# Kernel optimization log

Measured on AMD Instinct MI355X. Metric: run time of the kernel, lower is better.

## Reference

```python
import jax, jax.numpy as jnp
import numpy as np

# Model dims (Gemma-class)
B, T, HID = 1, 3072, 2048
H, KH, D = 16, 8, 128          # q heads, kv heads, head_dim
WIN = 1024                     # sliding window
EPS = 1e-6
SEQ = 1536                     # two packed sequences of length 1536


def _rms(x, w):
    # torch nn.RMSNorm: x * rsqrt(mean(x^2) + eps) [* weight]
    var = jnp.mean(x * x, axis=-1, keepdims=True)
    y = x * jax.lax.rsqrt(var + EPS)
    return y if w is None else y * w


def _rotate_half(x):
    x1, x2 = jnp.split(x, 2, axis=-1)
    return jnp.concatenate([-x2, x1], axis=-1)


def _rope(x, cos, sin):
    # x: [B,T,h,D]; cos/sin: [B,T,rd] -> unsqueeze head dim (matches cos.unsqueeze(2))
    c = cos[:, :, None, :]
    s = sin[:, :, None, :]
    rd = cos.shape[-1]
    xr, xp = x[..., :rd], x[..., rd:]
    xr = xr * c + _rotate_half(xr) * s
    return jnp.concatenate([xr, xp], axis=-1)


def _build_mask(cu_seqlens):
    # causal & within sliding window & same packed sequence (matches _sliding_mask)
    idx = jnp.arange(T)
    seg = jnp.searchsorted(cu_seqlens, idx, side='right') - 1
    i = idx[:, None]
    j = idx[None, :]
    return (i >= j) & ((i - j) < WIN) & (seg[:, None] == seg[None, :])


def _attn_layer(x, wq, qn, k, v, wo, cos, sin, mask):
    # x: [B,T,HID]; k,v: [T,KH,D] (possibly shared from an earlier layer)
    q = _rope(_rms((x @ wq).reshape(B, T, H, D), qn), cos, sin).reshape(T, H, D)
    rep = H // k.shape[1]
    kk = jnp.repeat(k, rep, axis=1)   # GQA: repeat_interleave over head dim
    vv = jnp.repeat(v, rep, axis=1)
    s = jnp.einsum('qhd,khd->hqk', q, kk)          # scale = 1.0 (as in source)
    s = jnp.where(mask, s, jnp.asarray(-1e30, s.dtype))
    p = jax.nn.softmax(s, axis=-1)
    o = jnp.einsum('hqk,khd->qhd', p, vv).reshape(B, T, H * D)
    return o @ wo


def setup_inputs() -> dict:
    key = jax.random.key(0)
    ks = jax.random.split(key, 10)
    hidden_states = jax.random.normal(ks[0], (B, T, HID), jnp.float32)
    # RoPE tables with per-packed-sequence position resets
    pos = jnp.concatenate([jnp.arange(SEQ), jnp.arange(SEQ)]).astype(jnp.float32)
    inv = 1.0 / (10000.0 ** (jnp.arange(0, D, 2, dtype=jnp.float32) / D))
    fr = pos[:, None] * inv[None, :]
    emb = jnp.concatenate([fr, fr], axis=-1)     # [T, D]
    cos = jnp.cos(emb)[None]                     # [1, T, D]
    sin = jnp.sin(emb)[None]
    w = lambda k, sh: 0.02 * jax.random.normal(k, sh, jnp.float32)
    return {
        'hidden_states': hidden_states,
        'cos': cos, 'sin': sin,
        'wq0': w(ks[1], (HID, H * D)), 'wk0': w(ks[2], (HID, KH * D)),
        'wv0': w(ks[3], (HID, KH * D)), 'wo0': w(ks[4], (H * D, HID)),
        'qn0': 1.0 + 0.01 * jax.random.normal(ks[5], (D,), jnp.float32),
        'kn0': 1.0 + 0.01 * jax.random.normal(ks[6], (D,), jnp.float32),
        'wq1': w(ks[7], (HID, H * D)), 'wo1': w(ks[8], (H * D, HID)),
        'qn1': 1.0 + 0.01 * jax.random.normal(ks[9], (D,), jnp.float32),
        'cu_seqlens': jnp.array([0, SEQ, T], dtype=jnp.int32),
    }


def reference(hidden_states, cos, sin, wq0, wk0, wv0, wo0, qn0, kn0, wq1, wo1, qn1, cu_seqlens):
    mask = _build_mask(cu_seqlens)
    # Layer 0: source layer -> computes and stores K/V
    k = _rope(_rms((hidden_states @ wk0).reshape(B, T, KH, D), kn0), cos, sin).reshape(T, KH, D)
    v = _rms((hidden_states @ wv0).reshape(B, T, KH, D), None).reshape(T, KH, D)
    out0 = _attn_layer(hidden_states, wq0, qn0, k, v, wo0, cos, sin, mask)
    # Layer 1: KV-shared layer -> reuses layer 0's K/V (skips k/v projections)
    out1 = _attn_layer(out0, wq1, qn1, k, v, wo1, cos, sin, mask)
    return out1
```

## Files before the change

kernel.cpp:

```cpp
#include <hip/hip_runtime.h>
#include <hip/hip_bf16.h>

#define T_TOK 3072
#define HIDDEN 2048
#define NHQ 16
#define NHKV 8
#define DH 128
#define WINDOW 1024

typedef __attribute__((ext_vector_type(4))) float f32x4;
typedef __attribute__((ext_vector_type(8))) short bf16x8;
typedef __attribute__((ext_vector_type(8))) unsigned short ushort8;
typedef __attribute__((ext_vector_type(4))) unsigned short ushort4v;

__device__ __forceinline__ unsigned short f2bf(float f) {
  union { float fv; unsigned u; } v; v.fv = f;
  unsigned r = v.u + 0x7fffu + ((v.u >> 16) & 1u);
  return (unsigned short)(r >> 16);
}
__device__ __forceinline__ float bf2f(unsigned short h) {
  union { unsigned u; float f; } v; v.u = ((unsigned)h) << 16;
  return v.f;
}
__device__ __forceinline__ void split2(float f, unsigned short& hi, unsigned short& lo) {
  hi = f2bf(f);
  lo = f2bf(f - bf2f(hi));
}

__global__ __launch_bounds__(256) void cvt_split(const float* __restrict__ x,
                                                 unsigned short* __restrict__ yh,
                                                 unsigned short* __restrict__ yl, int n) {
  int i = (blockIdx.x * 256 + threadIdx.x) * 4;
  if (i >= n) return;
  f32x4 v = *(const f32x4*)(x + i);
  ushort4v oh, ol;
#pragma unroll
  for (int j = 0; j < 4; ++j) {
    unsigned short h, l;
    split2(v[j], h, l);
    oh[j] = h; ol[j] = l;
  }
  *(ushort4v*)(yh + i) = oh;
  *(ushort4v*)(yl + i) = ol;
}

__global__ __launch_bounds__(256) void transpose_w_split(const float* __restrict__ W,
                                                         unsigned short* __restrict__ Wth,
                                                         unsigned short* __restrict__ Wtl,
                                                         int K, int N) {
  __shared__ float tile[32][33];
  int bn = blockIdx.x * 32, bk = blockIdx.y * 32;
  int tx = threadIdx.x & 31, ty = threadIdx.x >> 5;
#pragma unroll
  for (int i = 0; i < 4; ++i)
    tile[ty + i * 8][tx] = W[(size_t)(bk + ty + i * 8) * N + bn + tx];
  __syncthreads();
#pragma unroll
  for (int i = 0; i < 4; ++i) {
    unsigned short h, l;
    split2(tile[tx][ty + i * 8], h, l);
    Wth[(size_t)(bn + ty + i * 8) * K + bk + tx] = h;
    if (Wtl) Wtl[(size_t)(bn + ty + i * 8) * K + bk + tx] = l;
  }
}

__global__ __launch_bounds__(256) void transpose_u16(const unsigned short* __restrict__ src,
                                                     unsigned short* __restrict__ dst,
                                                     int R, int C) {
  __shared__ unsigned short tile[32][33];
  int bc = blockIdx.x * 32, br = blockIdx.y * 32;
  int tx = threadIdx.x & 31, ty = threadIdx.x >> 5;
#pragma unroll
  for (int i = 0; i < 4; ++i)
    tile[ty + i * 8][tx] = src[(size_t)(br + ty + i * 8) * C + bc + tx];
  __syncthreads();
#pragma unroll
  for (int i = 0; i < 4; ++i)
    dst[(size_t)(bc + ty + i * 8) * R + br + tx] = tile[tx][ty + i * 8];
}

#define GSLOT(lane) ((((lane) & 3) + 4 - (((lane) >> 3) & 3)) & 3)

__global__ __launch_bounds__(256) void gemm3_128(const unsigned short* __restrict__ Ah,
                                                 const unsigned short* __restrict__ Al,
                                                 const unsigned short* __restrict__ Bh,
                                                 const unsigned short* __restrict__ Bl,
                                                 float* __restrict__ Cq,
                                                 float* __restrict__ Ckv,
                                                 int strd, int M, int N, int K) {
  __shared__ unsigned short ah_lds[128 * 32];
  __shared__ unsigned short al_lds[128 * 32];
  __shared__ unsigned short bh_lds[128 * 32];
  __shared__ unsigned short bl_lds[128 * 32];
  const int tid = threadIdx.x, lane = tid & 63, wave = tid >> 6;
  const int wr = (wave >> 1) * 64, wc = (wave & 1) * 64;
  const int g = lane >> 4, r16 = lane & 15;
  int nwg = gridDim.x * gridDim.y;
  int id = blockIdx.y * gridDim.x + blockIdx.x;
  int nid = (id & 7) * (nwg >> 3) + (id >> 3);
  const int bm = nid % gridDim.x, bn = nid / gridDim.x;
  f32x4 acc[4][4];
#pragma unroll
  for (int i = 0; i < 4; ++i)
#pragma unroll
    for (int j = 0; j < 4; ++j) acc[i][j] = (f32x4){0.f, 0.f, 0.f, 0.f};

  const unsigned short* AhB = Ah + (size_t)bm * 128 * K;
  const unsigned short* AlB = Al + (size_t)bm * 128 * K;
  const unsigned short* BhB = Bh + (size_t)bn * 128 * K;
  const unsigned short* BlB = Bl + (size_t)bn * 128 * K;

  const int slg = GSLOT(lane) * 8;
  const int sr = ((r16 >> 1) & 3);

  for (int kt = 0; kt < K; kt += 32) {
    __syncthreads();
#pragma unroll
    for (int c = 0; c < 2; ++c) {
      size_t goff = (size_t)(wave * 32 + c * 16 + (lane >> 2)) * K + kt + slg;
      int loff = (wave * 2 + c) * 512;
      __builtin_amdgcn_global_load_lds(
          (const __attribute__((address_space(1))) unsigned int*)(AhB + goff),
          (__attribute__((address_space(3))) unsigned int*)(ah_lds + loff), 16, 0, 0);
      __builtin_amdgcn_global_load_lds(
          (const __attribute__((address_space(1))) unsigned int*)(AlB + goff),
          (__attribute__((address_space(3))) unsigned int*)(al_lds + loff), 16, 0, 0);
      __builtin_amdgcn_global_load_lds(
          (const __attribute__((address_space(1))) unsigned int*)(BhB + goff),
          (__attribute__((address_space(3))) unsigned int*)(bh_lds + loff), 16, 0, 0);
      __builtin_amdgcn_global_load_lds(
          (const __attribute__((address_space(1))) unsigned int*)(BlB + goff),
          (__attribute__((address_space(3))) unsigned int*)(bl_lds + loff), 16, 0, 0);
    }
    __syncthreads();
    bf16x8 ahf[4], alf[4], bhf[4], blf[4];
#pragma unroll
    for (int i = 0; i < 4; ++i) {
      int sa = ((g + sr) & 3) * 8;
      ahf[i] = *(const bf16x8*)&ah_lds[(wr + i * 16 + r16) * 32 + sa];
      alf[i] = *(const bf16x8*)&al_lds[(wr + i * 16 + r16) * 32 + sa];
      bhf[i] = *(const bf16x8*)&bh_lds[(wc + i * 16 + r16) * 32 + sa];
      blf[i] = *(const bf16x8*)&bl_lds[(wc + i * 16 + r16) * 32 + sa];
    }
#pragma unroll
    for (int i = 0; i < 4; ++i)
#pragma unroll
      for (int j = 0; j < 4; ++j) {
        acc[i][j] = __builtin_amdgcn_mfma_f32_16x16x32_bf16(ahf[i], bhf[j], acc[i][j], 0, 0, 0);
        acc[i][j] = __builtin_amdgcn_mfma_f32_16x16x32_bf16(ahf[i], blf[j], acc[i][j], 0, 0, 0);
        acc[i][j] = __builtin_amdgcn_mfma_f32_16x16x32_bf16(alf[i], bhf[j], acc[i][j], 0, 0, 0);
      }
  }

#pragma unroll
  for (int i = 0; i < 4; ++i) {
    int row = bm * 128 + wr + i * 16 + g * 4;
#pragma unroll
    for (int j = 0; j < 4; ++j) {
      int colg = bn * 128 + wc + j * 16 + r16;
      float* Cb; int cc;
      if (colg < 2048) { Cb = Cq; cc = colg; } else { Cb = Ckv; cc = colg - 2048; }
#pragma unroll
      for (int r = 0; r < 4; ++r)
        Cb[(size_t)(row + r) * strd + cc] = acc[i][j][r];
    }
  }
}

template <int OUT>
__global__ __launch_bounds__(256) void gemm3_96(const unsigned short* __restrict__ Ah,
                                                const unsigned short* __restrict__ Al,
                                                const unsigned short* __restrict__ Bh,
                                                const unsigned short* __restrict__ Bl,
                                                float* __restrict__ Cf,
                                                unsigned short* __restrict__ Ch,
                                                unsigned short* __restrict__ Cl,
                                                int M, int N, int K) {
  __shared__ unsigned short ah_lds[96 * 32];
  __shared__ unsigned short al_lds[96 * 32];
  __shared__ unsigned short bh_lds[128 * 32];
  __shared__ unsigned short bl_lds[128 * 32];
  const int tid = threadIdx.x, lane = tid & 63, wave = tid >> 6;
  const int wr = (wave >> 1) * 48, wc = (wave & 1) * 64;
  const int g = lane >> 4, r16 = lane & 15;
  int nwg = gridDim.x * gridDim.y;
  int id = blockIdx.y * gridDim.x + blockIdx.x;
  int nid = (id & 7) * (nwg >> 3) + (id >> 3);
  const int bm = nid % gridDim.x, bn = nid / gridDim.x;
  f32x4 acc[3][4];
#pragma unroll
  for (int i = 0; i < 3; ++i)
#pragma unroll
    for (int j = 0; j < 4; ++j) acc[i][j] = (f32x4){0.f, 0.f, 0.f, 0.f};

  const unsigned short* AhB = Ah + (size_t)bm * 96 * K;
  const unsigned short* AlB = Al + (size_t)bm * 96 * K;
  const unsigned short* BhB = Bh + (size_t)bn * 128 * K;
  const unsigned short* BlB = Bl + (size_t)bn * 128 * K;

  const int slg = GSLOT(lane) * 8;
  const int sr = ((r16 >> 1) & 3);

  for (int kt = 0; kt < K; kt += 32) {
    __syncthreads();
    {
      int c = wave;
      size_t goff = (size_t)(c * 16 + (lane >> 2)) * K + kt + slg;
      __builtin_amdgcn_global_load_lds(
          (const __attribute__((address_space(1))) unsigned int*)(AhB + goff),
          (__attribute__((address_space(3))) unsigned int*)(ah_lds + c * 512), 16, 0, 0);
      __builtin_amdgcn_global_load_lds(
          (const __attribute__((address_space(1))) unsigned int*)(AlB + goff),
          (__attribute__((address_space(3))) unsigned int*)(al_lds + c * 512), 16, 0, 0);
      if (wave < 2) {
        int c2 = 4 + wave;
        size_t goff2 = (size_t)(c2 * 16 + (lane >> 2)) * K + kt + slg;
        __builtin_amdgcn_global_load_lds(
            (const __attribute__((address_space(1))) unsigned int*)(AhB + goff2),
            (__attribute__((address_space(3))) unsigned int*)(ah_lds + c2 * 512), 16, 0, 0);
        __builtin_amdgcn_global_load_lds(
            (const __attribute__((address_space(1))) unsigned int*)(AlB + goff2),
            (__attribute__((address_space(3))) unsigned int*)(al_lds + c2 * 512), 16, 0, 0);
      }
    }
#pragma unroll
    for (int c = 0; c < 2; ++c) {
      size_t goff = (size_t)(wave * 32 + c * 16 + (lane >> 2)) * K + kt + slg;
      int loff = (wave * 2 + c) * 512;
      __builtin_amdgcn_global_load_lds(
          (const __attribute__((address_space(1))) unsigned int*)(BhB + goff),
          (__attribute__((address_space(3))) unsigned int*)(bh_lds + loff), 16, 0, 0);
      __builtin_amdgcn_global_load_lds(
          (const __attribute__((address_space(1))) unsigned int*)(BlB + goff),
          (__attribute__((address_space(3))) unsigned int*)(bl_lds + loff), 16, 0, 0);
    }
    __syncthreads();
    bf16x8 ahf[3], alf[3], bhf[4], blf[4];
    int sa = ((g + sr) & 3) * 8;
#pragma unroll
    for (int i = 0; i < 3; ++i) {
      ahf[i] = *(const bf16x8*)&ah_lds[(wr + i * 16 + r16) * 32 + sa];
      alf[i] = *(const bf16x8*)&al_lds[(wr + i * 16 + r16) * 32 + sa];
    }
#pragma unroll
    for (int j = 0; j < 4; ++j) {
      bhf[j] = *(const bf16x8*)&bh_lds[(wc + j * 16 + r16) * 32 + sa];
      blf[j] = *(const bf16x8*)&bl_lds[(wc + j * 16 + r16) * 32 + sa];
    }
#pragma unroll
    for (int i = 0; i < 3; ++i)
#pragma unroll
      for (int j = 0; j < 4; ++j) {
        acc[i][j] = __builtin_amdgcn_mfma_f32_16x16x32_bf16(ahf[i], bhf[j], acc[i][j], 0, 0, 0);
        acc[i][j] = __builtin_amdgcn_mfma_f32_16x16x32_bf16(ahf[i], blf[j], acc[i][j], 0, 0, 0);
        acc[i][j] = __builtin_amdgcn_mfma_f32_16x16x32_bf16(alf[i], bhf[j], acc[i][j], 0, 0, 0);
      }
  }

#pragma unroll
  for (int i = 0; i < 3; ++i) {
    int row = bm * 96 + wr + i * 16 + g * 4;
#pragma unroll
    for (int j = 0; j < 4; ++j) {
      int col = bn * 128 + wc + j * 16 + r16;
#pragma unroll
      for (int r = 0; r < 4; ++r) {
        if (OUT == 0) {
          Cf[(size_t)(row + r) * N + col] = acc[i][j][r];
        } else {
          unsigned short h, l;
          split2(acc[i][j][r], h, l);
          Ch[(size_t)(row + r) * N + col] = h;
          Cl[(size_t)(row + r) * N + col] = l;
        }
      }
    }
  }
}

__global__ __launch_bounds__(256) void gemm1_96(const unsigned short* __restrict__ Ah,
                                                const unsigned short* __restrict__ Bh,
                                                float* __restrict__ Cf,
                                                int M, int N, int K) {
  __shared__ unsigned short ah_lds[96 * 32];
  __shared__ unsigned short bh_lds[128 * 32];
  const int tid = threadIdx.x, lane = tid & 63, wave = tid >> 6;
  const int wr = (wave >> 1) * 48, wc = (wave & 1) * 64;
  const int g = lane >> 4, r16 = lane & 15;
  int nwg = gridDim.x * gridDim.y;
  int id = blockIdx.y * gridDim.x + blockIdx.x;
  int nid = (id & 7) * (nwg >> 3) + (id >> 3);
  const int bm = nid % gridDim.x, bn = nid / gridDim.x;
  f32x4 acc[3][4];
#pragma unroll
  for (int i = 0; i < 3; ++i)
#pragma unroll
    for (int j = 0; j < 4; ++j) acc[i][j] = (f32x4){0.f, 0.f, 0.f, 0.f};

  const unsigned short* AhB = Ah + (size_t)bm * 96 * K;
  const unsigned short* BhB = Bh + (size_t)bn * 128 * K;

  const int slg = GSLOT(lane) * 8;
  const int sr = ((r16 >> 1) & 3);

  for (int kt = 0; kt < K; kt += 32) {
    __syncthreads();
    {
      int c = wave;
      size_t goff = (size_t)(c * 16 + (lane >> 2)) * K + kt + slg;
      __builtin_amdgcn_global_load_lds(
          (const __attribute__((address_space(1))) unsigned int*)(AhB + goff),
          (__attribute__((address_space(3))) unsigned int*)(ah_lds + c * 512), 16, 0, 0);
      if (wave < 2) {
        int c2 = 4 + wave;
        size_t goff2 = (size_t)(c2 * 16 + (lane >> 2)) * K + kt + slg;
        __builtin_amdgcn_global_load_lds(
            (const __attribute__((address_space(1))) unsigned int*)(AhB + goff2),
            (__attribute__((address_space(3))) unsigned int*)(ah_lds + c2 * 512), 16, 0, 0);
      }
    }
#pragma unroll
    for (int c = 0; c < 2; ++c) {
      size_t goff = (size_t)(wave * 32 + c * 16 + (lane >> 2)) * K + kt + slg;
      __builtin_amdgcn_global_load_lds(
          (const __attribute__((address_space(1))) unsigned int*)(BhB + goff),
          (__attribute__((address_space(3))) unsigned int*)(bh_lds + (wave * 2 + c) * 512), 16, 0, 0);
    }
    __syncthreads();
    bf16x8 ahf[3], bhf[4];
    int sa = ((g + sr) & 3) * 8;
#pragma unroll
    for (int i = 0; i < 3; ++i)
      ahf[i] = *(const bf16x8*)&ah_lds[(wr + i * 16 + r16) * 32 + sa];
#pragma unroll
    for (int j = 0; j < 4; ++j)
      bhf[j] = *(const bf16x8*)&bh_lds[(wc + j * 16 + r16) * 32 + sa];
#pragma unroll
    for (int i = 0; i < 3; ++i)
#pragma unroll
      for (int j = 0; j < 4; ++j)
        acc[i][j] = __builtin_amdgcn_mfma_f32_16x16x32_bf16(ahf[i], bhf[j], acc[i][j], 0, 0, 0);
  }

#pragma unroll
  for (int i = 0; i < 3; ++i) {
    int row = bm * 96 + wr + i * 16 + g * 4;
#pragma unroll
    for (int j = 0; j < 4; ++j) {
      int col = bn * 128 + wc + j * 16 + r16;
#pragma unroll
      for (int r = 0; r < 4; ++r)
        Cf[(size_t)(row + r) * N + col] = acc[i][j][r];
    }
  }
}

__global__ __launch_bounds__(256) void rms_rope_split(const float* __restrict__ X,
                                                      const float* __restrict__ w,
                                                      const float* __restrict__ cosp,
                                                      const float* __restrict__ sinp,
                                                      unsigned short* __restrict__ outh,
                                                      unsigned short* __restrict__ outl,
                                                      int NH, int doRope, int XS, int XO) {
  int row = blockIdx.x * 4 + (threadIdx.x >> 6);
  int lane = threadIdx.x & 63;
  int t = row / NH, hh_ = row % NH;
  const float* x = X + (size_t)t * XS + XO + (size_t)hh_ * DH;
  float x1 = x[lane], x2 = x[lane + 64];
  float ss = x1 * x1 + x2 * x2;
#pragma unroll
  for (int m = 1; m < 64; m <<= 1) ss += __shfl_xor(ss, m, 64);
  float inv = rsqrtf(ss * (1.0f / 128.0f) + 1e-6f);
  float y1 = x1 * inv, y2 = x2 * inv;
  if (w) { y1 *= w[lane]; y2 *= w[lane + 64]; }
  if (doRope) {
    float c1 = cosp[t * DH + lane], s1 = sinp[t * DH + lane];
    float c2 = cosp[t * DH + lane + 64], s2 = sinp[t * DH + lane + 64];
    float o1 = y1 * c1 - y2 * s1;
    float o2 = y2 * c2 + y1 * s2;
    y1 = o1; y2 = o2;
  }
  unsigned short h, l;
  split2(y1, h, l);
  outh[(size_t)row * DH + lane] = h;
  if (outl) outl[(size_t)row * DH + lane] = l;
  split2(y2, h, l);
  outh[(size_t)row * DH + lane + 64] = h;
  if (outl) outl[(size_t)row * DH + lane + 64] = l;
}

template <int WRITE_LO>
__global__ __launch_bounds__(384) void attn3(const float* __restrict__ Qf,
                                             const float* __restrict__ qnw,
                                             const float* __restrict__ cosp,
                                             const float* __restrict__ sinp,
                                             const unsigned short* __restrict__ Kh,
                                             const unsigned short* __restrict__ Kl,
                                             const unsigned short* __restrict__ Vth,
                                             unsigned short* __restrict__ Oh,
                                             unsigned short* __restrict__ Ol,
                                             const int* __restrict__ cu, int ncu) {
  __shared__ unsigned short kh_lds[32][136];
  __shared__ unsigned short kl_lds[32][136];
  __shared__ unsigned short vh_lds[144][40];
  __shared__ unsigned short ph_lds[6][16][40];

  int id = blockIdx.y * gridDim.x + blockIdx.x;
  int nid = (id & 7) * 64 + (id >> 3);
  const int qt = nid & 31, h = nid >> 5;
  const int qbase = qt * 96;
  const int kvh = h >> 1;
  const int tid = threadIdx.x, lane = tid & 63, wave = tid >> 6;
  const int g = lane >> 4, r16 = lane & 15;

  for (int i = tid; i < 16 * 40; i += 384) {
    int rr = i / 40, cc = i % 40;
    vh_lds[128 + rr][cc] = (rr == 0) ? (unsigned short)0x3F80 : (unsigned short)0;
  }

  bf16x8 aqh[4], aql[4];
  {
    int q_r = qbase + wave * 16 + r16;
    const float* xq = Qf + (size_t)q_r * HIDDEN + h * DH;
    float xv[4][8];
    float ss = 0.f;
#pragma unroll
    for (int ks = 0; ks < 4; ++ks) {
      f32x4 a = *(const f32x4*)(xq + ks * 32 + g * 8);
      f32x4 b = *(const f32x4*)(xq + ks * 32 + g * 8 + 4);
#pragma unroll
      for (int j = 0; j < 4; ++j) { xv[ks][j] = a[j]; xv[ks][4 + j] = b[j]; }
#pragma unroll
      for (int j = 0; j < 8; ++j) ss += xv[ks][j] * xv[ks][j];
    }
    ss += __shfl_xor(ss, 16, 64);
    ss += __shfl_xor(ss, 32, 64);
    float inv = rsqrtf(ss * (1.0f / 128.0f) + 1e-6f);
    float y[4][8];
#pragma unroll
    for (int ks = 0; ks < 4; ++ks) {
      f32x4 w0 = *(const f32x4*)(qnw + ks * 32 + g * 8);
      f32x4 w1 = *(const f32x4*)(qnw + ks * 32 + g * 8 + 4);
#pragma unroll
      for (int j = 0; j < 4; ++j) {
        y[ks][j] = xv[ks][j] * inv * w0[j];
        y[ks][4 + j] = xv[ks][4 + j] * inv * w1[j];
      }
    }
    const float* cb = cosp + (size_t)q_r * DH;
    const float* sb = sinp + (size_t)q_r * DH;
#pragma unroll
    for (int ks = 0; ks < 4; ++ks) {
      bf16x8 th, tl;
#pragma unroll
      for (int j2 = 0; j2 < 2; ++j2) {
        int col = ks * 32 + g * 8 + j2 * 4;
        f32x4 cv = *(const f32x4*)(cb + col);
        f32x4 sv = *(const f32x4*)(sb + col);
#pragma unroll
        for (int j = 0; j < 4; ++j) {
          float o;
          if (ks < 2) o = y[ks][j2 * 4 + j] * cv[j] - y[ks + 2][j2 * 4 + j] * sv[j];
          else        o = y[ks][j2 * 4 + j] * cv[j] + y[ks - 2][j2 * 4 + j] * sv[j];
          unsigned short hx, lx;
          split2(o, hx, lx);
          th[j2 * 4 + j] = (short)hx;
          tl[j2 * 4 + j] = (short)lx;
        }
      }
      aqh[ks] = th; aql[ks] = tl;
    }
  }

  int ssr[4];
#pragma unroll
  for (int r = 0; r < 4; ++r) {
    int q_r = qbase + wave * 16 + g * 4 + r;
    int s = 0;
    for (int i = 1; i < ncu; ++i) { int v = cu[i]; if (v <= q_r) s = v; }
    ssr[r] = s;
  }
  int ss_base = 0;
  for (int i = 1; i < ncu; ++i) { int v = cu[i]; if (v <= qbase) ss_base = v; }

  float m_r[4] = {-1e30f, -1e30f, -1e30f, -1e30f};
  f32x4 oacc[8];
#pragma unroll
  for (int db = 0; db < 8; ++db) oacc[db] = (f32x4){0.f, 0.f, 0.f, 0.f};
  f32x4 oaccL = (f32x4){0.f, 0.f, 0.f, 0.f};

  int lo = qbase - WINDOW + 1;
  if (lo < ss_base) lo = ss_base;
  if (lo < 0) lo = 0;
  int kt0 = lo & ~31;
  int ktend = qbase + 95;

  const bool stager = tid < 256;
  const int krow = (tid & 255) >> 3, kc = tid & 7;
  const int vd = (tid & 255) >> 1, vhalf = (tid & 1) * 16;
  const int qmin = qbase + wave * 16;
  const int sw0 = ((kc + 2 * (krow & 15)) & 15) * 16;
  const int sw1 = ((kc + 8 + 2 * (krow & 15)) & 15) * 16;

  ushort8 rkh0, rkh1, rkl0, rkl1, rvh0, rvh1;
  auto loadTile = [&](int kt) {
    if (!stager) return;
    size_t goff = ((size_t)(kt + krow) * NHKV + kvh) * DH + kc * 8;
    rkh0 = *(const ushort8*)(Kh + goff);
    rkh1 = *(const ushort8*)(Kh + goff + 64);
    rkl0 = *(const ushort8*)(Kl + goff);
    rkl1 = *(const ushort8*)(Kl + goff + 64);
    size_t voff = ((size_t)kvh * DH + vd) * T_TOK + kt + vhalf;
    rvh0 = *(const ushort8*)(Vth + voff);
    rvh1 = *(const ushort8*)(Vth + voff + 8);
  };
  auto writeTile = [&]() {
    if (!stager) return;
    char* kbh = (char*)&kh_lds[krow][0];
    char* kbl = (char*)&kl_lds[krow][0];
    *(ushort8*)(kbh + sw0) = rkh0;
    *(ushort8*)(kbh + sw1) = rkh1;
    *(ushort8*)(kbl + sw0) = rkl0;
    *(ushort8*)(kbl + sw1) = rkl1;
    *(ushort8*)&vh_lds[vd][vhalf] = rvh0;
    *(ushort8*)&vh_lds[vd][vhalf + 8] = rvh1;
  };

  loadTile(kt0);
  writeTile();
  __syncthreads();

  for (int kt = kt0; kt <= ktend; kt += 32) {
    const bool hasNext = (kt + 32 <= ktend);
    if (hasNext) loadTile(kt + 32);

    f32x4 s0 = (f32x4){0.f, 0.f, 0.f, 0.f}, s1 = (f32x4){0.f, 0.f, 0.f, 0.f};
    {
      const char* kb0h = (const char*)&kh_lds[r16][0];
      const char* kb1h = (const char*)&kh_lds[16 + r16][0];
      const char* kb0l = (const char*)&kl_lds[r16][0];
      const char* kb1l = (const char*)&kl_lds[16 + r16][0];
#pragma unroll
      for (int ks = 0; ks < 4; ++ks) {
        int sl = ((ks * 4 + g + 2 * r16) & 15) * 16;
        bf16x8 bh0 = *(const bf16x8*)(kb0h + sl);
        bf16x8 bh1 = *(const bf16x8*)(kb1h + sl);
        bf16x8 bl0 = *(const bf16x8*)(kb0l + sl);
        bf16x8 bl1 = *(const bf16x8*)(kb1l + sl);
        s0 = __builtin_amdgcn_mfma_f32_16x16x32_bf16(aqh[ks], bh0, s0, 0, 0, 0);
        s0 = __builtin_amdgcn_mfma_f32_16x16x32_bf16(aqh[ks], bl0, s0, 0, 0, 0);
        s0 = __builtin_amdgcn_mfma_f32_16x16x32_bf16(aql[ks], bh0, s0, 0, 0, 0);
        s1 = __builtin_amdgcn_mfma_f32_16x16x32_bf16(aqh[ks], bh1, s1, 0, 0, 0);
        s1 = __builtin_amdgcn_mfma_f32_16x16x32_bf16(aqh[ks], bl1, s1, 0, 0, 0);
        s1 = __builtin_amdgcn_mfma_f32_16x16x32_bf16(aql[ks], bh1, s1, 0, 0, 0);
      }
    }

    float sv0_[4], sv1_[4], mt_[4];
    bool ok0_[4], ok1_[4];
    bool interior = (kt + 31 <= qmin) && (kt >= qmin + 16 - WINDOW) &&
                    __all(kt >= ssr[3]);
    if (interior) {
#pragma unroll
      for (int r = 0; r < 4; ++r) {
        ok0_[r] = ok1_[r] = true;
        sv0_[r] = s0[r]; sv1_[r] = s1[r];
      }
    } else {
#pragma unroll
      for (int r = 0; r < 4; ++r) {
        int q_r = qmin + g * 4 + r;
        int k0 = kt + r16, k1 = k0 + 16;
        ok0_[r] = (k0 <= q_r) && (k0 > q_r - WINDOW) && (k0 >= ssr[r]);
        ok1_[r] = (k1 <= q_r) && (k1 > q_r - WINDOW) && (k1 >= ssr[r]);
        sv0_[r] = ok0_[r] ? s0[r] : -1e30f;
        sv1_[r] = ok1_[r] ? s1[r] : -1e30f;
      }
    }
#pragma unroll
    for (int r = 0; r < 4; ++r) {
      float mt = fmaxf(sv0_[r], sv1_[r]);
#pragma unroll
      for (int mm = 1; mm < 16; mm <<= 1) mt = fmaxf(mt, __shfl_xor(mt, mm, 64));
      mt_[r] = mt;
    }
    float grow = fmaxf(fmaxf(mt_[0] - m_r[0], mt_[1] - m_r[1]),
                       fmaxf(mt_[2] - m_r[2], mt_[3] - m_r[3]));
    if (!__all(grow <= 8.0f)) {
#pragma unroll
      for (int r = 0; r < 4; ++r) {
        float mnew = fmaxf(m_r[r], mt_[r]);
        float alpha = __expf(m_r[r] - mnew);
        m_r[r] = mnew;
#pragma unroll
        for (int db = 0; db < 8; ++db) oacc[db][r] *= alpha;
        oaccL[r] *= alpha;
      }
    }
#pragma unroll
    for (int r = 0; r < 4; ++r) {
      float p0v = ok0_[r] ? __expf(sv0_[r] - m_r[r]) : 0.f;
      float p1v = ok1_[r] ? __expf(sv1_[r] - m_r[r]) : 0.f;
      ph_lds[wave][g * 4 + r][r16] = f2bf(p0v);
      ph_lds[wave][g * 4 + r][16 + r16] = f2bf(p1v);
    }

    bf16x8 pah = *(const bf16x8*)&ph_lds[wave][r16][g * 8];
#pragma unroll
    for (int db = 0; db < 8; ++db) {
      bf16x8 vfh = *(const bf16x8*)&vh_lds[db * 16 + r16][g * 8];
      oacc[db] = __builtin_amdgcn_mfma_f32_16x16x32_bf16(pah, vfh, oacc[db], 0, 0, 0);
    }
    {
      bf16x8 vfo = *(const bf16x8*)&vh_lds[128 + r16][g * 8];
      oaccL = __builtin_amdgcn_mfma_f32_16x16x32_bf16(pah, vfo, oaccL, 0, 0, 0);
    }

    __syncthreads();
    if (hasNext) writeTile();
    __syncthreads();
  }

#pragma unroll
  for (int r = 0; r < 4; ++r) {
    int q_r = qbase + wave * 16 + g * 4 + r;
    float lsum = __shfl(oaccL[r], lane & 48, 64);
    float invl = 1.f / lsum;
#pragma unroll
    for (int db = 0; db < 8; ++db) {
      float ov = oacc[db][r] * invl;
      unsigned short hh, ll;
      split2(ov, hh, ll);
      Oh[(size_t)q_r * (NHQ * DH) + h * DH + db * 16 + r16] = hh;
      if (WRITE_LO) Ol[(size_t)q_r * (NHQ * DH) + h * DH + db * 16 + r16] = ll;
    }
  }
}

extern "C" void kernel_launch(void* const* d_in, const int* in_sizes, int n_in,
                              void* d_out, int out_size, void* d_ws, size_t ws_size,
                              hipStream_t stream) {
  const float* hidden = (const float*)d_in[0];
  const float* cosp   = (const float*)d_in[1];
  const float* sinp   = (const float*)d_in[2];
  const float* wq0    = (const float*)d_in[3];
  const float* wk0    = (const float*)d_in[4];
  const float* wv0    = (const float*)d_in[5];
  const float* wo0    = (const float*)d_in[6];
  const float* qn0    = (const float*)d_in[7];
  const float* kn0    = (const float*)d_in[8];
  const float* wq1    = (const float*)d_in[9];
  const float* wo1    = (const float*)d_in[10];
  const float* qn1    = (const float*)d_in[11];
  const int*   cu     = (const int*)d_in[12];
  int ncu = in_sizes[12];
  (void)n_in; (void)out_size; (void)ws_size;

  const int nX = T_TOK * HIDDEN;
  const int KVN = NHKV * DH;

  char* p = (char*)d_ws;
  auto alloc = [&](size_t bytes) { char* r = p; p += (bytes + 255) & ~255ull; return r; };

  float*          c32q  = (float*)alloc((size_t)T_TOK * HIDDEN * 4);
  float*          c32kv = (float*)alloc((size_t)T_TOK * HIDDEN * 4);
  unsigned short* xh    = (unsigned short*)alloc((size_t)T_TOK * HIDDEN * 2);
  unsigned short* xl    = (unsigned short*)alloc((size_t)T_TOK * HIDDEN * 2);
  unsigned short* wth   = (unsigned short*)alloc((size_t)2 * HIDDEN * HIDDEN * 2);
  unsigned short* wtl   = (unsigned short*)alloc((size_t)2 * HIDDEN * HIDDEN * 2);
  unsigned short* kh    = (unsigned short*)alloc((size_t)T_TOK * KVN * 2);
  unsigned short* kl    = (unsigned short*)alloc((size_t)T_TOK * KVN * 2);
  unsigned short* vh    = (unsigned short*)alloc((size_t)T_TOK * KVN * 2);
  unsigned short* vth   = (unsigned short*)alloc((size_t)T_TOK * KVN * 2);
  unsigned short* x1h   = (unsigned short*)alloc((size_t)T_TOK * HIDDEN * 2);
  unsigned short* x1l   = (unsigned short*)alloc((size_t)T_TOK * HIDDEN * 2);

  cvt_split<<<nX / 1024, 256, 0, stream>>>(hidden, xh, xl, nX);

  transpose_w_split<<<dim3(HIDDEN / 32, HIDDEN / 32), 256, 0, stream>>>(wq0, wth, wtl, HIDDEN, HIDDEN);
  transpose_w_split<<<dim3(KVN / 32, HIDDEN / 32), 256, 0, stream>>>(
      wk0, wth + (size_t)HIDDEN * HIDDEN, wtl + (size_t)HIDDEN * HIDDEN, HIDDEN, KVN);
  transpose_w_split<<<dim3(KVN / 32, HIDDEN / 32), 256, 0, stream>>>(
      wv0, wth + (size_t)(HIDDEN + KVN) * HIDDEN, wtl + (size_t)(HIDDEN + KVN) * HIDDEN, HIDDEN, KVN);

  gemm3_128<<<dim3(T_TOK / 128, 4096 / 128), 256, 0, stream>>>(
      xh, xl, wth, wtl, c32q, c32kv, HIDDEN, T_TOK, 4096, HIDDEN);

  rms_rope_split<<<T_TOK * NHKV / 4, 256, 0, stream>>>(c32kv, kn0, cosp, sinp, kh, kl, NHKV, 1, HIDDEN, 0);
  rms_rope_split<<<T_TOK * NHKV / 4, 256, 0, stream>>>(c32kv, nullptr, cosp, sinp, vh, nullptr, NHKV, 0, HIDDEN, KVN);

  transpose_u16<<<dim3(KVN / 32, T_TOK / 32), 256, 0, stream>>>(vh, vth, T_TOK, KVN);

  attn3<1><<<dim3(32, 16), 384, 0, stream>>>(c32q, qn0, cosp, sinp, kh, kl, vth, xh, xl, cu, ncu);

  transpose_w_split<<<dim3(HIDDEN / 32, HIDDEN / 32), 256, 0, stream>>>(wo0, wth, wtl, HIDDEN, HIDDEN);
  gemm3_96<2><<<dim3(T_TOK / 96, HIDDEN / 128), 256, 0, stream>>>(
      xh, xl, wth, wtl, nullptr, x1h, x1l, T_TOK, HIDDEN, HIDDEN);

  transpose_w_split<<<dim3(HIDDEN / 32, HIDDEN / 32), 256, 0, stream>>>(wq1, wth, wtl, HIDDEN, HIDDEN);
  gemm3_96<0><<<dim3(T_TOK / 96, HIDDEN / 128), 256, 0, stream>>>(
      x1h, x1l, wth, wtl, c32kv, nullptr, nullptr, T_TOK, HIDDEN, HIDDEN);

  attn3<0><<<dim3(32, 16), 384, 0, stream>>>(c32kv, qn1, cosp, sinp, kh, kl, vth, xh, nullptr, cu, ncu);

  transpose_w_split<<<dim3(HIDDEN / 32, HIDDEN / 32), 256, 0, stream>>>(wo1, wth, nullptr, HIDDEN, HIDDEN);
  gemm1_96<<<dim3(T_TOK / 96, HIDDEN / 128), 256, 0, stream>>>(xh, wth, (float*)d_out, T_TOK, HIDDEN, HIDDEN);
}
```

Measured before the change: 680.2 us.

## Fold wo0 and wq1 into one combined weight to skip a token GEMM

Computes the product Wo0·Wq1 as a 2048x2048 weight-by-weight GEMM, so layer 1's query comes from the attention output with one token-sized GEMM instead of two (out0 projection, then q1 projection). The three QKV weight transposes are merged into one launch, and the K and V RMS kernels are merged into one. This removes one T×2048×2048 three-pass split GEMM at the cost of a 2048³ GEMM plus extra rounding when the folded weight is stored as a hi/lo split. It also reuses c32q as scratch space for the combined weight.

```diff
diff --git a/kernel.cpp b/kernel.cpp
--- a/kernel.cpp
+++ b/kernel.cpp
@@ -7,6 +7,7 @@
 #define NHKV 8
 #define DH 128
 #define WINDOW 1024
+#define KVN 1024
 
 typedef __attribute__((ext_vector_type(4))) float f32x4;
 typedef __attribute__((ext_vector_type(8))) short bf16x8;
@@ -44,6 +45,34 @@
   *(ushort4v*)(yl + i) = ol;
 }
 
+__global__ __launch_bounds__(256) void transpose_qkv(const float* __restrict__ wq0,
+                                                     const float* __restrict__ wk0,
+                                                     const float* __restrict__ wv0,
+                                                     unsigned short* __restrict__ Wth,
+                                                     unsigned short* __restrict__ Wtl) {
+  __shared__ float tile[32][33];
+  const int K = HIDDEN;
+  int id = blockIdx.x;
+  const float* W; int N, local; size_t dstoff;
+  if (id < 4096)      { W = wq0; N = 2048; local = id;        dstoff = 0; }
+  else if (id < 6144) { W = wk0; N = 1024; local = id - 4096; dstoff = (size_t)2048 * K; }
+  else                { W = wv0; N = 1024; local = id - 6144; dstoff = (size_t)3072 * K; }
+  int ntc = N / 32;
+  int bn = (local % ntc) * 32, bk = (local / ntc) * 32;
+  int tx = threadIdx.x & 31, ty = threadIdx.x >> 5;
+#pragma unroll
+  for (int i = 0; i < 4; ++i)
+    tile[ty + i * 8][tx] = W[(size_t)(bk + ty + i * 8) * N + bn + tx];
+  __syncthreads();
+#pragma unroll
+  for (int i = 0; i < 4; ++i) {
+    unsigned short h, l;
+    split2(tile[tx][ty + i * 8], h, l);
+    Wth[dstoff + (size_t)(bn + ty + i * 8) * K + bk + tx] = h;
+    Wtl[dstoff + (size_t)(bn + ty + i * 8) * K + bk + tx] = l;
+  }
+}
+
 __global__ __launch_bounds__(256) void transpose_w_split(const float* __restrict__ W,
                                                          unsigned short* __restrict__ Wth,
                                                          unsigned short* __restrict__ Wtl,
@@ -81,12 +110,15 @@
 
 #define GSLOT(lane) ((((lane) & 3) + 4 - (((lane) >> 3) & 3)) & 3)
 
+template <int OUT>
 __global__ __launch_bounds__(256) void gemm3_128(const unsigned short* __restrict__ Ah,
                                                  const unsigned short* __restrict__ Al,
                                                  const unsigned short* __restrict__ Bh,
                                                  const unsigned short* __restrict__ Bl,
                                                  float* __restrict__ Cq,
                                                  float* __restrict__ Ckv,
+                                                 unsigned short* __restrict__ Ch,
+                                                 unsigned short* __restrict__ Cl,
                                                  int strd, int M, int N, int K) {
   __shared__ unsigned short ah_lds[128 * 32];
   __shared__ unsigned short al_lds[128 * 32];
@@ -134,9 +166,9 @@
     }
     __syncthreads();
     bf16x8 ahf[4], alf[4], bhf[4], blf[4];
+    int sa = ((g + sr) & 3) * 8;
 #pragma unroll
     for (int i = 0; i < 4; ++i) {
-      int sa = ((g + sr) & 3) * 8;
       ahf[i] = *(const bf16x8*)&ah_lds[(wr + i * 16 + r16) * 32 + sa];
       alf[i] = *(const bf16x8*)&al_lds[(wr + i * 16 + r16) * 32 + sa];
       bhf[i] = *(const bf16x8*)&bh_lds[(wc + i * 16 + r16) * 32 + sa];
@@ -158,23 +190,30 @@
 #pragma unroll
     for (int j = 0; j < 4; ++j) {
       int colg = bn * 128 + wc + j * 16 + r16;
-      float* Cb; int cc;
-      if (colg < 2048) { Cb = Cq; cc = colg; } else { Cb = Ckv; cc = colg - 2048; }
-#pragma unroll
-      for (int r = 0; r < 4; ++r)
-        Cb[(size_t)(row + r) * strd + cc] = acc[i][j][r];
-    }
-  }
-}
-
-template <int OUT>
+      if (OUT == 0) {
+        float* Cb; int cc;
+        if (colg < 2048) { Cb = Cq; cc = colg; } else { Cb = Ckv; cc = colg - 2048; }
+#pragma unroll
+        for (int r = 0; r < 4; ++r)
+          Cb[(size_t)(row + r) * strd + cc] = acc[i][j][r];
+      } else {
+#pragma unroll
+        for (int r = 0; r < 4; ++r) {
+          unsigned short h, l;
+          split2(acc[i][j][r], h, l);
+          Ch[(size_t)(row + r) * N + colg] = h;
+          Cl[(size_t)(row + r) * N + colg] = l;
+        }
+      }
+    }
+  }
+}
+
 __global__ __launch_bounds__(256) void gemm3_96(const unsigned short* __restrict__ Ah,
                                                 const unsigned short* __restrict__ Al,
                                                 const unsigned short* __restrict__ Bh,
                                                 const unsigned short* __restrict__ Bl,
                                                 float* __restrict__ Cf,
-                                                unsigned short* __restrict__ Ch,
-                                                unsigned short* __restrict__ Cl,
                                                 int M, int N, int K) {
   __shared__ unsigned short ah_lds[96 * 32];
   __shared__ unsigned short al_lds[96 * 32];
@@ -264,16 +303,8 @@
     for (int j = 0; j < 4; ++j) {
       int col = bn * 128 + wc + j * 16 + r16;
 #pragma unroll
-      for (int r = 0; r < 4; ++r) {
-        if (OUT == 0) {
-          Cf[(size_t)(row + r) * N + col] = acc[i][j][r];
-        } else {
-          unsigned short h, l;
-          split2(acc[i][j][r], h, l);
-          Ch[(size_t)(row + r) * N + col] = h;
-          Cl[(size_t)(row + r) * N + col] = l;
-        }
-      }
+      for (int r = 0; r < 4; ++r)
+        Cf[(size_t)(row + r) * N + col] = acc[i][j][r];
     }
   }
 }
@@ -355,38 +386,43 @@
   }
 }
 
-__global__ __launch_bounds__(256) void rms_rope_split(const float* __restrict__ X,
-                                                      const float* __restrict__ w,
-                                                      const float* __restrict__ cosp,
-                                                      const float* __restrict__ sinp,
-                                                      unsigned short* __restrict__ outh,
-                                                      unsigned short* __restrict__ outl,
-                                                      int NH, int doRope, int XS, int XO) {
-  int row = blockIdx.x * 4 + (threadIdx.x >> 6);
+__global__ __launch_bounds__(256) void rms_kv(const float* __restrict__ X,
+                                              const float* __restrict__ kn,
+                                              const float* __restrict__ cosp,
+                                              const float* __restrict__ sinp,
+                                              unsigned short* __restrict__ kh,
+                                              unsigned short* __restrict__ kl,
+                                              unsigned short* __restrict__ vh) {
+  const int half = T_TOK * NHKV / 4;
+  bool isV = (int)blockIdx.x >= half;
+  int bid = isV ? blockIdx.x - half : blockIdx.x;
+  int row = bid * 4 + (threadIdx.x >> 6);
   int lane = threadIdx.x & 63;
-  int t = row / NH, hh_ = row % NH;
-  const float* x = X + (size_t)t * XS + XO + (size_t)hh_ * DH;
+  int t = row >> 3, hh_ = row & 7;
+  const float* x = X + (size_t)t * HIDDEN + (isV ? KVN : 0) + (size_t)hh_ * DH;
   float x1 = x[lane], x2 = x[lane + 64];
   float ss = x1 * x1 + x2 * x2;
 #pragma unroll
   for (int m = 1; m < 64; m <<= 1) ss += __shfl_xor(ss, m, 64);
   float inv = rsqrtf(ss * (1.0f / 128.0f) + 1e-6f);
   float y1 = x1 * inv, y2 = x2 * inv;
-  if (w) { y1 *= w[lane]; y2 *= w[lane + 64]; }
-  if (doRope) {
+  if (!isV) {
+    y1 *= kn[lane]; y2 *= kn[lane + 64];
     float c1 = cosp[t * DH + lane], s1 = sinp[t * DH + lane];
     float c2 = cosp[t * DH + lane + 64], s2 = sinp[t * DH + lane + 64];
     float o1 = y1 * c1 - y2 * s1;
     float o2 = y2 * c2 + y1 * s2;
-    y1 = o1; y2 = o2;
-  }
-  unsigned short h, l;
-  split2(y1, h, l);
-  outh[(size_t)row * DH + lane] = h;
-  if (outl) outl[(size_t)row * DH + lane] = l;
-  split2(y2, h, l);
-  outh[(size_t)row * DH + lane + 64] = h;
-  if (outl) outl[(size_t)row * DH + lane + 64] = l;
+    unsigned short h, l;
+    split2(o1, h, l);
+    kh[(size_t)row * DH + lane] = h;
+    kl[(size_t)row * DH + lane] = l;
+    split2(o2, h, l);
+    kh[(size_t)row * DH + lane + 64] = h;
+    kl[(size_t)row * DH + lane + 64] = l;
+  } else {
+    vh[(size_t)row * DH + lane] = f2bf(y1);
+    vh[(size_t)row * DH + lane + 64] = f2bf(y2);
+  }
 }
 
 template <int WRITE_LO>
@@ -657,7 +693,6 @@
   (void)n_in; (void)out_size; (void)ws_size;
 
   const int nX = T_TOK * HIDDEN;
-  const int KVN = NHKV * DH;
 
   char* p = (char*)d_ws;
   auto alloc = [&](size_t bytes) { char* r = p; p += (bytes + 255) & ~255ull; return r; };
@@ -672,37 +707,41 @@
   unsigned short* kl    = (unsigned short*)alloc((size_t)T_TOK * KVN * 2);
   unsigned short* vh    = (unsigned short*)alloc((size_t)T_TOK * KVN * 2);
   unsigned short* vth   = (unsigned short*)alloc((size_t)T_TOK * KVN * 2);
-  unsigned short* x1h   = (unsigned short*)alloc((size_t)T_TOK * HIDDEN * 2);
-  unsigned short* x1l   = (unsigned short*)alloc((size_t)T_TOK * HIDDEN * 2);
+
+  unsigned short* wo0sh = wth;
+  unsigned short* wo0sl = wtl;
+  unsigned short* wq1th = wth + (size_t)HIDDEN * HIDDEN;
+  unsigned short* wq1tl = wtl + (size_t)HIDDEN * HIDDEN;
+  unsigned short* W01th = (unsigned short*)c32q;
+  unsigned short* W01tl = W01th + (size_t)HIDDEN * HIDDEN;
+  unsigned short* wo1t  = wth;
 
   cvt_split<<<nX / 1024, 256, 0, stream>>>(hidden, xh, xl, nX);
 
-  transpose_w_split<<<dim3(HIDDEN / 32, HIDDEN / 32), 256, 0, stream>>>(wq0, wth, wtl, HIDDEN, HIDDEN);
-  transpose_w_split<<<dim3(KVN / 32, HIDDEN / 32), 256, 0, stream>>>(
-      wk0, wth + (size_t)HIDDEN * HIDDEN, wtl + (size_t)HIDDEN * HIDDEN, HIDDEN, KVN);
-  transpose_w_split<<<dim3(KVN / 32, HIDDEN / 32), 256, 0, stream>>>(
-      wv0, wth + (size_t)(HIDDEN + KVN) * HIDDEN, wtl + (size_t)(HIDDEN + KVN) * HIDDEN, HIDDEN, KVN);
-
-  gemm3_128<<<dim3(T_TOK / 128, 4096 / 128), 256, 0, stream>>>(
-      xh, xl, wth, wtl, c32q, c32kv, HIDDEN, T_TOK, 4096, HIDDEN);
-
-  rms_rope_split<<<T_TOK * NHKV / 4, 256, 0, stream>>>(c32kv, kn0, cosp, sinp, kh, kl, NHKV, 1, HIDDEN, 0);
-  rms_rope_split<<<T_TOK * NHKV / 4, 256, 0, stream>>>(c32kv, nullptr, cosp, sinp, vh, nullptr, NHKV, 0, HIDDEN, KVN);
+  transpose_qkv<<<8192, 256, 0, stream>>>(wq0, wk0, wv0, wth, wtl);
+
+  gemm3_128<0><<<dim3(T_TOK / 128, 4096 / 128), 256, 0, stream>>>(
+      xh, xl, wth, wtl, c32q, c32kv, nullptr, nullptr, HIDDEN, T_TOK, 4096, HIDDEN);
+
+  cvt_split<<<(HIDDEN * HIDDEN) / 1024, 256, 0, stream>>>(wo0, wo0sh, wo0sl, HIDDEN * HIDDEN);
+
+  transpose_w_split<<<dim3(HIDDEN / 32, HIDDEN / 32), 256, 0, stream>>>(wq1, wq1th, wq1tl, HIDDEN, HIDDEN);
+
+  rms_kv<<<2 * T_TOK * NHKV / 4, 256, 0, stream>>>(c32kv, kn0, cosp, sinp, kh, kl, vh);
 
   transpose_u16<<<dim3(KVN / 32, T_TOK / 32), 256, 0, stream>>>(vh, vth, T_TOK, KVN);
 
   attn3<1><<<dim3(32, 16), 384, 0, stream>>>(c32q, qn0, cosp, sinp, kh, kl, vth, xh, xl, cu, ncu);
 
-  transpose_w_split<<<dim3(HIDDEN / 32, HIDDEN / 32), 256, 0, stream>>>(wo0, wth, wtl, HIDDEN, HIDDEN);
-  gemm3_96<2><<<dim3(T_TOK / 96, HIDDEN / 128), 256, 0, stream>>>(
-      xh, xl, wth, wtl, nullptr, x1h, x1l, T_TOK, HIDDEN, HIDDEN);
-
-  transpose_w_split<<<dim3(HIDDEN / 32, HIDDEN / 32), 256, 0, stream>>>(wq1, wth, wtl, HIDDEN, HIDDEN);
-  gemm3_96<0><<<dim3(T_TOK / 96, HIDDEN / 128), 256, 0, stream>>>(
-      x1h, x1l, wth, wtl, c32kv, nullptr, nullptr, T_TOK, HIDDEN, HIDDEN);
+  gemm3_128<2><<<dim3(HIDDEN / 128, HIDDEN / 128), 256, 0, stream>>>(
+      wq1th, wq1tl, wo0sh, wo0sl, nullptr, nullptr, W01th, W01tl, HIDDEN, HIDDEN, HIDDEN, HIDDEN);
+
+  gemm3_96<<<dim3(T_TOK / 96, HIDDEN / 128), 256, 0, stream>>>(
+      xh, xl, W01th, W01tl, c32kv, T_TOK, HIDDEN, HIDDEN);
+
+  transpose_w_split<<<dim3(HIDDEN / 32, HIDDEN / 32), 256, 0, stream>>>(wo1, wo1t, nullptr, HIDDEN, HIDDEN);
 
   attn3<0><<<dim3(32, 16), 384, 0, stream>>>(c32kv, qn1, cosp, sinp, kh, kl, vth, xh, nullptr, cu, ncu);
 
-  transpose_w_split<<<dim3(HIDDEN / 32, HIDDEN / 32), 256, 0, stream>>>(wo1, wth, nullptr, HIDDEN, HIDDEN);
-  gemm1_96<<<dim3(T_TOK / 96, HIDDEN / 128), 256, 0, stream>>>(xh, wth, (float*)d_out, T_TOK, HIDDEN, HIDDEN);
-}
+  gemm1_96<<<dim3(T_TOK / 96, HIDDEN / 128), 256, 0, stream>>>(xh, wo1t, (float*)d_out, T_TOK, HIDDEN, HIDDEN);
+}
```

After: 666.6 us. -2.0%, faster.
